# Kernel tuning notes

Hardware: AMD Instinct MI355X
Metric: run time of the kernel (lower is better)

Reference implementation:

```python
import jax, jax.numpy as jnp
import numpy as np

D_MODEL = 2048
NUM_HEADS = 16
HEAD_DIM = D_MODEL // NUM_HEADS  # 128


def setup_inputs() -> dict:
    key = jax.random.key(0)
    ks = jax.random.split(key, 9)
    s = 0.02
    x = jax.random.normal(ks[0], (2, 2048, D_MODEL), dtype=jnp.float32)
    Wq = jax.random.normal(ks[1], (D_MODEL, D_MODEL), dtype=jnp.float32) * s
    bq = jnp.zeros((D_MODEL,), dtype=jnp.float32)
    Wk = jax.random.normal(ks[2], (D_MODEL, HEAD_DIM), dtype=jnp.float32) * s
    bk = jnp.zeros((HEAD_DIM,), dtype=jnp.float32)
    Wv = jax.random.normal(ks[3], (D_MODEL, HEAD_DIM), dtype=jnp.float32) * s
    bv = jnp.zeros((HEAD_DIM,), dtype=jnp.float32)
    Wo = jax.random.normal(ks[4], (D_MODEL, D_MODEL), dtype=jnp.float32) * s
    bo = jnp.zeros((D_MODEL,), dtype=jnp.float32)
    return {"x": x, "Wq": Wq, "bq": bq, "Wk": Wk, "bk": bk,
            "Wv": Wv, "bv": bv, "Wo": Wo, "bo": bo}


def reference(x, Wq, bq, Wk, bk, Wv, bv, Wo, bo):
    B, S, _ = x.shape
    # projections
    q = (x @ Wq + bq).reshape(B, S, NUM_HEADS, HEAD_DIM)  # [B,S,H,d]
    k = x @ Wk + bk  # [B,S,d] shared across heads (MQA)
    v = x @ Wv + bv  # [B,S,d]
    scale = 1.0 / jnp.sqrt(jnp.float32(HEAD_DIM))
    # QK^T with shared K: [B,H,Sq,Sk]
    scores = jnp.einsum('bqhd,bkd->bhqk', q, k) * scale
    attn = jax.nn.softmax(scores, axis=-1)
    # AV with shared V: [B,H,Sq,d]
    out = jnp.einsum('bhqk,bkd->bqhd', attn, v).reshape(B, S, D_MODEL)
    return out @ Wo + bo
```

## Files before the change

kernel.cpp:

```cpp
#include <hip/hip_runtime.h>


typedef __attribute__((ext_vector_type(8))) short short8;
typedef __attribute__((ext_vector_type(4))) float f32x4;
typedef __attribute__((ext_vector_type(4))) unsigned int uint4v;

__device__ __forceinline__ unsigned short f2bf(float f) {
  unsigned int u = __float_as_uint(f);
  u += 0x7FFF + ((u >> 16) & 1);
  return (unsigned short)(u >> 16);
}

__device__ __forceinline__ unsigned int pk2(float a, float b) {
  return (unsigned int)f2bf(a) | ((unsigned int)f2bf(b) << 16);
}

__device__ __forceinline__ void gll16(const void* g, void* lds) {
  __builtin_amdgcn_global_load_lds(
      (const __attribute__((address_space(1))) unsigned int*)g,
      (__attribute__((address_space(3))) unsigned int*)lds, 16, 0, 0);
}

__global__ __launch_bounds__(256) void cvtk(const float* __restrict__ in,
                                            unsigned short* __restrict__ out, int n4) {
  int i = blockIdx.x * blockDim.x + threadIdx.x;
  int stride = gridDim.x * blockDim.x;
  for (; i < n4; i += stride) {
    float4 v = reinterpret_cast<const float4*>(in)[i];
    ushort4 o;
    o.x = f2bf(v.x); o.y = f2bf(v.y); o.z = f2bf(v.z); o.w = f2bf(v.w);
    reinterpret_cast<ushort4*>(out)[i] = o;
  }
}

__global__ __launch_bounds__(256) void tcvt2(const float* __restrict__ W0, const float* __restrict__ W1,
                                             unsigned short* __restrict__ D0, unsigned short* __restrict__ D1,
                                             int K, int N) {
  const float* W = blockIdx.z ? W1 : W0;
  unsigned short* Wt = blockIdx.z ? D1 : D0;
  __shared__ float tile[32][33];
  int n0 = blockIdx.x * 32, k0 = blockIdx.y * 32;
  int tx = threadIdx.x, ty = threadIdx.y;
  #pragma unroll
  for (int i = 0; i < 32; i += 8)
    tile[ty + i][tx] = W[(size_t)(k0 + ty + i) * N + n0 + tx];
  __syncthreads();
  #pragma unroll
  for (int i = 0; i < 32; i += 8)
    Wt[(size_t)(n0 + ty + i) * K + k0 + tx] = f2bf(tile[tx][ty + i]);
}

template <int MODE>
__global__ __launch_bounds__(256)
void gemm_nt(const unsigned short* __restrict__ A, const unsigned short* __restrict__ Bt,
             const float* __restrict__ b0, const float* __restrict__ b1,
             const float* __restrict__ b2,
             void* __restrict__ C, unsigned short* __restrict__ C2,
             unsigned short* __restrict__ C3, int M, int N, int K, float cmul) {
  __shared__ unsigned short lA[128 * 64];
  __shared__ unsigned short lB[128 * 64];
  const int t = threadIdx.x;
  const int lane = t & 63;
  const int w = t >> 6;
  const int wr = w >> 1, wc = w & 1;
  const int r15 = lane & 15, g4 = lane >> 4;
  const int tileM = blockIdx.y * 128;
  const int tileN = blockIdx.x * 128;

  f32x4 acc[4][4];
  #pragma unroll
  for (int i = 0; i < 4; i++)
    #pragma unroll
    for (int j = 0; j < 4; j++) acc[i][j] = (f32x4){0.f, 0.f, 0.f, 0.f};

  const int nkt = K >> 6;
  for (int kt = 0; kt < nkt; ++kt) {
    const int k0 = kt * 64;
    #pragma unroll
    for (int i = 0; i < 4; ++i) {
      int flat = i * 256 + t;
      int row = flat >> 3, gc = flat & 7;
      unsigned lb = (unsigned)(i * 256 + w * 64) * 16;
      gll16(A  + (size_t)(tileM + row) * K + k0 + gc * 8, (char*)lA + lb);
      gll16(Bt + (size_t)(tileN + row) * K + k0 + gc * 8, (char*)lB + lb);
    }
    __syncthreads();
    #pragma unroll
    for (int kk = 0; kk < 2; ++kk) {
      short8 af[4], bf[4];
      #pragma unroll
      for (int mt = 0; mt < 4; ++mt)
        af[mt] = *reinterpret_cast<const short8*>(&lA[(wr * 64 + mt * 16 + r15) * 64 + kk * 32 + g4 * 8]);
      #pragma unroll
      for (int nt = 0; nt < 4; ++nt)
        bf[nt] = *reinterpret_cast<const short8*>(&lB[(wc * 64 + nt * 16 + r15) * 64 + kk * 32 + g4 * 8]);
      #pragma unroll
      for (int mt = 0; mt < 4; ++mt)
        #pragma unroll
        for (int nt = 0; nt < 4; ++nt)
          acc[mt][nt] = __builtin_amdgcn_mfma_f32_16x16x32_bf16(af[mt], bf[nt], acc[mt][nt], 0, 0, 0);
    }
    __syncthreads();
  }

  #pragma unroll
  for (int mt = 0; mt < 4; ++mt) {
    #pragma unroll
    for (int nt = 0; nt < 4; ++nt) {
      int col = tileN + wc * 64 + nt * 16 + r15;
      #pragma unroll
      for (int r = 0; r < 4; ++r) {
        int row = tileM + wr * 64 + mt * 16 + g4 * 4 + r;
        float v = acc[mt][nt][r];
        if (MODE == 1) {
          ((float*)C)[(size_t)row * N + col] = v + b0[col];
        } else {
          if (col < 2048) {
            ((unsigned short*)C)[(size_t)row * 2048 + col] = f2bf((v + b0[col]) * cmul);
          } else if (col < 2176) {
            int dd = col - 2048;
            C2[(size_t)row * 128 + dd] = f2bf(v + b1[dd]);
          } else {
            int dd = col - 2176;
            int bb = row >> 11, s = row & 2047;
            C3[((size_t)bb * 128 + dd) * 2048 + s] = f2bf(v + b2[dd]);
          }
        }
      }
    }
  }
}

__global__ __launch_bounds__(256)
void flash_mqa(const unsigned short* __restrict__ qb, const unsigned short* __restrict__ kb,
               const unsigned short* __restrict__ vt, unsigned short* __restrict__ ob) {
  __shared__ unsigned short lK[2][64 * 128];
  __shared__ unsigned short lV[2][128 * 64];
  __shared__ unsigned short lP[4][16 * 64];

  const int t = threadIdx.x;
  const int lane = t & 63;
  const int w = t >> 6;
  const int r15 = lane & 15, g4 = lane >> 4;
  const int qt = blockIdx.x, hy = blockIdx.y, b = blockIdx.z;
  const int q0 = qt * 64 + w * 16;

  short8 qf[2][4];
  const size_t qrow = (size_t)(b * 2048 + q0 + r15);
  #pragma unroll
  for (int hh = 0; hh < 2; ++hh)
    #pragma unroll
    for (int kk = 0; kk < 4; ++kk)
      qf[hh][kk] = *reinterpret_cast<const short8*>(
          &qb[qrow * 2048 + (hy * 2 + hh) * 128 + kk * 32 + g4 * 8]);

  f32x4 oacc[2][8];
  #pragma unroll
  for (int hh = 0; hh < 2; ++hh)
    #pragma unroll
    for (int i = 0; i < 8; i++) oacc[hh][i] = (f32x4){0.f, 0.f, 0.f, 0.f};
  float m_q[2] = {-1e30f, -1e30f}, l_q[2] = {0.f, 0.f};

  const unsigned short* kbase = kb + (size_t)b * 2048 * 128;
  const unsigned short* vbase = vt + (size_t)b * 128 * 2048;

  auto stage = [&](int buf, int kv0) {
    #pragma unroll
    for (int i = 0; i < 4; ++i) {
      int flat = i * 256 + t;
      unsigned lb = (unsigned)(i * 256 + w * 64) * 16;
      { int row = flat >> 4, gc = flat & 15;
        gll16(kbase + (size_t)(kv0 + row) * 128 + ((gc ^ (row & 15)) << 3), (char*)lK[buf] + lb); }
      { int row = flat >> 3, gc = flat & 7;
        gll16(vbase + (size_t)row * 2048 + kv0 + ((gc ^ (row & 7)) << 3), (char*)lV[buf] + lb); }
    }
  };

  stage(0, 0);
  int cur = 0;
  for (int it = 0; it < 32; ++it) {
    if (it < 31) {
      stage(cur ^ 1, (it + 1) * 64);
      asm volatile("s_waitcnt vmcnt(8)" ::: "memory");
    } else {
      asm volatile("s_waitcnt vmcnt(0)" ::: "memory");
    }
    __builtin_amdgcn_s_barrier();
    asm volatile("" ::: "memory");

    const unsigned short* cK = lK[cur];
    const unsigned short* cV = lV[cur];

    #pragma unroll
    for (int hh = 0; hh < 2; ++hh) {
      f32x4 s[4];
      #pragma unroll
      for (int ct = 0; ct < 4; ct++) s[ct] = (f32x4){0.f, 0.f, 0.f, 0.f};
      #pragma unroll
      for (int kk = 0; kk < 4; ++kk) {
        #pragma unroll
        for (int ct = 0; ct < 4; ++ct) {
          const int krow = ct * 16 + r15;
          const int kg = (kk * 4 + g4) ^ (krow & 15);
          short8 kf = *reinterpret_cast<const short8*>(&cK[krow * 128 + kg * 8]);
          s[ct] = __builtin_amdgcn_mfma_f32_16x16x32_bf16(kf, qf[hh][kk], s[ct], 0, 0, 0);
        }
      }

      float mx = s[0][0];
      #pragma unroll
      for (int ct = 0; ct < 4; ++ct)
        #pragma unroll
        for (int r = 0; r < 4; ++r) mx = fmaxf(mx, s[ct][r]);
      mx = fmaxf(mx, __shfl_xor(mx, 16));
      mx = fmaxf(mx, __shfl_xor(mx, 32));
      if (__any(mx > m_q[hh] + 11.5416f)) {
        float mn = fmaxf(m_q[hh], mx);
        float rf = exp2f(m_q[hh] - mn);
        m_q[hh] = mn;
        l_q[hh] *= rf;
        #pragma unroll
        for (int ot = 0; ot < 8; ++ot)
          #pragma unroll
          for (int r = 0; r < 4; ++r) oacc[hh][ot][r] *= rf;
      }
      #pragma unroll
      for (int ct = 0; ct < 4; ++ct) {
        float p0 = exp2f(s[ct][0] - m_q[hh]);
        float p1 = exp2f(s[ct][1] - m_q[hh]);
        float p2 = exp2f(s[ct][2] - m_q[hh]);
        float p3 = exp2f(s[ct][3] - m_q[hh]);
        l_q[hh] += (p0 + p1) + (p2 + p3);
        const int gi = (ct * 4 + g4) ^ r15;
        *reinterpret_cast<uint2*>(&lP[w][r15 * 64 + gi * 4]) = make_uint2(pk2(p0, p1), pk2(p2, p3));
      }

      #pragma unroll
      for (int kk = 0; kk < 2; ++kk) {
        const int gA = (kk * 8 + g4 * 2) ^ r15;
        const int gB = (kk * 8 + g4 * 2 + 1) ^ r15;
        const uint2 wa = *reinterpret_cast<const uint2*>(&lP[w][r15 * 64 + gA * 4]);
        const uint2 wb = *reinterpret_cast<const uint2*>(&lP[w][r15 * 64 + gB * 4]);
        uint4v pw = {wa.x, wa.y, wb.x, wb.y};
        short8 pf = __builtin_bit_cast(short8, pw);
        #pragma unroll
        for (int ot = 0; ot < 8; ++ot) {
          const int vrow = ot * 16 + r15;
          const int vg = (kk * 4 + g4) ^ (vrow & 7);
          short8 vf = *reinterpret_cast<const short8*>(&cV[vrow * 64 + vg * 8]);
          oacc[hh][ot] = __builtin_amdgcn_mfma_f32_16x16x32_bf16(vf, pf, oacc[hh][ot], 0, 0, 0);
        }
      }
    }

    asm volatile("" ::: "memory");
    __builtin_amdgcn_s_barrier();
    cur ^= 1;
  }

  #pragma unroll
  for (int hh = 0; hh < 2; ++hh) {
    float l = l_q[hh];
    l += __shfl_xor(l, 16);
    l += __shfl_xor(l, 32);
    const float inv = 1.0f / l;
    const int row = q0 + r15;
    const size_t base = ((size_t)(b * 2048 + row)) * 2048 + (hy * 2 + hh) * 128;
    #pragma unroll
    for (int ot = 0; ot < 8; ++ot) {
      uint2 pw = make_uint2(pk2(oacc[hh][ot][0] * inv, oacc[hh][ot][1] * inv),
                            pk2(oacc[hh][ot][2] * inv, oacc[hh][ot][3] * inv));
      *reinterpret_cast<uint2*>(&ob[base + ot * 16 + g4 * 4]) = pw;
    }
  }
}

extern "C" void kernel_launch(void* const* d_in, const int* in_sizes, int n_in,
                              void* d_out, int out_size, void* d_ws, size_t ws_size,
                              hipStream_t stream) {
  const float* x  = (const float*)d_in[0];
  const float* Wq = (const float*)d_in[1];
  const float* bq = (const float*)d_in[2];
  const float* Wk = (const float*)d_in[3];
  const float* bk = (const float*)d_in[4];
  const float* Wv = (const float*)d_in[5];
  const float* bv = (const float*)d_in[6];
  const float* Wo = (const float*)d_in[7];
  const float* bo = (const float*)d_in[8];
  float* out = (float*)d_out;

  char* ws = (char*)d_ws;
  size_t off = 0;
  auto alloc = [&](size_t elems) {
    unsigned short* p = (unsigned short*)(ws + off);
    off += (elems * 2 + 255) & ~(size_t)255;
    return p;
  };
  unsigned short* xb    = alloc(8388608);
  unsigned short* qb    = alloc(8388608);
  unsigned short* ob    = alloc(8388608);
  unsigned short* wqkvt = alloc(4718592);
  unsigned short* wot   = alloc(4194304);
  unsigned short* kbuf  = alloc(524288);
  unsigned short* vtb   = alloc(524288);

  const float qscale = 0.08838834764831845f * 1.44269504088896f;

  dim3 tb(32, 8);
  cvtk<<<4096, 256, 0, stream>>>(x, xb, 2097152);
  tcvt2<<<dim3(64, 64, 2), tb, 0, stream>>>(Wq, Wo, wqkvt, wot, 2048, 2048);
  tcvt2<<<dim3(4, 64, 2),  tb, 0, stream>>>(Wk, Wv, wqkvt + (size_t)2048 * 2048,
                                            wqkvt + (size_t)2176 * 2048, 2048, 128);

  gemm_nt<3><<<dim3(18, 32), 256, 0, stream>>>(xb, wqkvt, bq, bk, bv,
                                               qb, kbuf, vtb, 4096, 2304, 2048, qscale);
  flash_mqa<<<dim3(32, 8, 2), 256, 0, stream>>>(qb, kbuf, vtb, ob);
  gemm_nt<1><<<dim3(16, 32), 256, 0, stream>>>(ob, wot, bo, nullptr, nullptr,
                                               out, nullptr, nullptr, 4096, 2048, 2048, 1.0f);
}
```

Baseline: 287.0 us.

## Double-buffer LDS tiles in GEMM to overlap global loads with MFMA

Turns the GEMM's single LDS buffers for A and B into two-stage ping-pong buffers. The next k-tile is issued via global_load_lds before computing on the current one, and each iteration ends with one vmcnt wait plus a barrier instead of two syncthreads. The aim is to hide global memory latency behind MFMA work. LDS use doubles to 64KB per block, which may lower occupancy. There is also a possible hazard: the next stage's loads could overwrite a buffer that slower waves are still reading.

After: 287.6 us. Within noise of the previous version (+0.2%).

```diff
diff --git a/kernel.cpp b/kernel.cpp
--- a/kernel.cpp
+++ b/kernel.cpp
@@ -57,8 +57,8 @@
              const float* __restrict__ b2,
              void* __restrict__ C, unsigned short* __restrict__ C2,
              unsigned short* __restrict__ C3, int M, int N, int K, float cmul) {
-  __shared__ unsigned short lA[128 * 64];
-  __shared__ unsigned short lB[128 * 64];
+  __shared__ unsigned short lA[2][128 * 64];
+  __shared__ unsigned short lB[2][128 * 64];
   const int t = threadIdx.x;
   const int lane = t & 63;
   const int w = t >> 6;
@@ -73,34 +73,52 @@
     #pragma unroll
     for (int j = 0; j < 4; j++) acc[i][j] = (f32x4){0.f, 0.f, 0.f, 0.f};
 
-  const int nkt = K >> 6;
-  for (int kt = 0; kt < nkt; ++kt) {
+  auto stage = [&](int buf, int kt) {
     const int k0 = kt * 64;
     #pragma unroll
     for (int i = 0; i < 4; ++i) {
       int flat = i * 256 + t;
       int row = flat >> 3, gc = flat & 7;
       unsigned lb = (unsigned)(i * 256 + w * 64) * 16;
-      gll16(A  + (size_t)(tileM + row) * K + k0 + gc * 8, (char*)lA + lb);
-      gll16(Bt + (size_t)(tileN + row) * K + k0 + gc * 8, (char*)lB + lb);
-    }
-    __syncthreads();
+      gll16(A  + (size_t)(tileM + row) * K + k0 + gc * 8, (char*)lA[buf] + lb);
+      gll16(Bt + (size_t)(tileN + row) * K + k0 + gc * 8, (char*)lB[buf] + lb);
+    }
+  };
+
+  const int nkt = K >> 6;
+  stage(0, 0);
+  asm volatile("s_waitcnt vmcnt(0)" ::: "memory");
+  __builtin_amdgcn_s_barrier();
+  asm volatile("" ::: "memory");
+
+  int cur = 0;
+  for (int kt = 0; kt < nkt; ++kt) {
+    if (kt + 1 < nkt) stage(cur ^ 1, kt + 1);
+
+    const unsigned short* cA = lA[cur];
+    const unsigned short* cB = lB[cur];
     #pragma unroll
     for (int kk = 0; kk < 2; ++kk) {
       short8 af[4], bf[4];
       #pragma unroll
       for (int mt = 0; mt < 4; ++mt)
-        af[mt] = *reinterpret_cast<const short8*>(&lA[(wr * 64 + mt * 16 + r15) * 64 + kk * 32 + g4 * 8]);
+        af[mt] = *reinterpret_cast<const short8*>(&cA[(wr * 64 + mt * 16 + r15) * 64 + kk * 32 + g4 * 8]);
       #pragma unroll
       for (int nt = 0; nt < 4; ++nt)
-        bf[nt] = *reinterpret_cast<const short8*>(&lB[(wc * 64 + nt * 16 + r15) * 64 + kk * 32 + g4 * 8]);
+        bf[nt] = *reinterpret_cast<const short8*>(&cB[(wc * 64 + nt * 16 + r15) * 64 + kk * 32 + g4 * 8]);
       #pragma unroll
       for (int mt = 0; mt < 4; ++mt)
         #pragma unroll
         for (int nt = 0; nt < 4; ++nt)
           acc[mt][nt] = __builtin_amdgcn_mfma_f32_16x16x32_bf16(af[mt], bf[nt], acc[mt][nt], 0, 0, 0);
     }
-    __syncthreads();
+
+    if (kt + 1 < nkt) {
+      asm volatile("s_waitcnt vmcnt(0)" ::: "memory");
+      __builtin_amdgcn_s_barrier();
+      asm volatile("" ::: "memory");
+    }
+    cur ^= 1;
   }
 
   #pragma unroll
```

## Merge prep kernels into one launch and enlarge GEMM tiles to 256x128

Applied to the files above, without the earlier changes.

Folds the x conversion and the two weight transpose-convert launches into a single prep kernel dispatched by block id, removing two kernel launches. The GEMM now uses 512-thread blocks covering 256x128 output tiles, so each B tile in LDS serves twice as many rows. It also replaces __syncthreads with an explicit vmcnt wait plus s_barrier. Larger tiles halve the grid and raise LDS use per block, which lowers the number of blocks and may reduce occupancy on a GPU with many CUs.

Result: no change. 284.8 us (-0.8%).

```diff
diff --git a/kernel.cpp b/kernel.cpp
--- a/kernel.cpp
+++ b/kernel.cpp
@@ -21,26 +21,46 @@
       (__attribute__((address_space(3))) unsigned int*)lds, 16, 0, 0);
 }
 
-__global__ __launch_bounds__(256) void cvtk(const float* __restrict__ in,
-                                            unsigned short* __restrict__ out, int n4) {
-  int i = blockIdx.x * blockDim.x + threadIdx.x;
-  int stride = gridDim.x * blockDim.x;
-  for (; i < n4; i += stride) {
-    float4 v = reinterpret_cast<const float4*>(in)[i];
-    ushort4 o;
-    o.x = f2bf(v.x); o.y = f2bf(v.y); o.z = f2bf(v.z); o.w = f2bf(v.w);
-    reinterpret_cast<ushort4*>(out)[i] = o;
-  }
-}
-
-__global__ __launch_bounds__(256) void tcvt2(const float* __restrict__ W0, const float* __restrict__ W1,
-                                             unsigned short* __restrict__ D0, unsigned short* __restrict__ D1,
-                                             int K, int N) {
-  const float* W = blockIdx.z ? W1 : W0;
-  unsigned short* Wt = blockIdx.z ? D1 : D0;
+__global__ __launch_bounds__(256)
+void prep(const float* __restrict__ x, unsigned short* __restrict__ xb,
+          const float* __restrict__ Wq, const float* __restrict__ Wo,
+          const float* __restrict__ Wk, const float* __restrict__ Wv,
+          unsigned short* __restrict__ wqkvt, unsigned short* __restrict__ wot) {
   __shared__ float tile[32][33];
-  int n0 = blockIdx.x * 32, k0 = blockIdx.y * 32;
-  int tx = threadIdx.x, ty = threadIdx.y;
+  const int bid = blockIdx.x;
+  const int t = threadIdx.x;
+
+  if (bid < 4096) {
+    int i = bid * 256 + t;
+    const int stride = 4096 * 256;
+    #pragma unroll
+    for (int rep = 0; rep < 2; ++rep, i += stride) {
+      float4 v = reinterpret_cast<const float4*>(x)[i];
+      ushort4 o;
+      o.x = f2bf(v.x); o.y = f2bf(v.y); o.z = f2bf(v.z); o.w = f2bf(v.w);
+      reinterpret_cast<ushort4*>(xb)[i] = o;
+    }
+    return;
+  }
+
+  const float* W;
+  unsigned short* Wt;
+  int K = 2048, N, bx, by;
+  if (bid < 12288) {
+    int r = bid - 4096;
+    int z = r >> 12, rr = r & 4095;
+    bx = rr & 63; by = rr >> 6; N = 2048;
+    W = z ? Wo : Wq;
+    Wt = z ? wot : wqkvt;
+  } else {
+    int r = bid - 12288;
+    int z = r >> 8, rr = r & 255;
+    bx = rr & 3; by = rr >> 2; N = 128;
+    W = z ? Wv : Wk;
+    Wt = wqkvt + (size_t)(z ? 2176 : 2048) * 2048;
+  }
+  const int tx = t & 31, ty = t >> 5;
+  const int n0 = bx * 32, k0 = by * 32;
   #pragma unroll
   for (int i = 0; i < 32; i += 8)
     tile[ty + i][tx] = W[(size_t)(k0 + ty + i) * N + n0 + tx];
@@ -51,20 +71,20 @@
 }
 
 template <int MODE>
-__global__ __launch_bounds__(256)
+__global__ __launch_bounds__(512, 4)
 void gemm_nt(const unsigned short* __restrict__ A, const unsigned short* __restrict__ Bt,
              const float* __restrict__ b0, const float* __restrict__ b1,
              const float* __restrict__ b2,
              void* __restrict__ C, unsigned short* __restrict__ C2,
              unsigned short* __restrict__ C3, int M, int N, int K, float cmul) {
-  __shared__ unsigned short lA[128 * 64];
+  __shared__ unsigned short lA[256 * 64];
   __shared__ unsigned short lB[128 * 64];
   const int t = threadIdx.x;
   const int lane = t & 63;
   const int w = t >> 6;
   const int wr = w >> 1, wc = w & 1;
   const int r15 = lane & 15, g4 = lane >> 4;
-  const int tileM = blockIdx.y * 128;
+  const int tileM = blockIdx.y * 256;
   const int tileN = blockIdx.x * 128;
 
   f32x4 acc[4][4];
@@ -78,13 +98,22 @@
     const int k0 = kt * 64;
     #pragma unroll
     for (int i = 0; i < 4; ++i) {
-      int flat = i * 256 + t;
+      int flat = i * 512 + t;
       int row = flat >> 3, gc = flat & 7;
-      unsigned lb = (unsigned)(i * 256 + w * 64) * 16;
-      gll16(A  + (size_t)(tileM + row) * K + k0 + gc * 8, (char*)lA + lb);
+      unsigned lb = (unsigned)(i * 512 + w * 64) * 16;
+      gll16(A + (size_t)(tileM + row) * K + k0 + gc * 8, (char*)lA + lb);
+    }
+    #pragma unroll
+    for (int i = 0; i < 2; ++i) {
+      int flat = i * 512 + t;
+      int row = flat >> 3, gc = flat & 7;
+      unsigned lb = (unsigned)(i * 512 + w * 64) * 16;
       gll16(Bt + (size_t)(tileN + row) * K + k0 + gc * 8, (char*)lB + lb);
     }
-    __syncthreads();
+    asm volatile("s_waitcnt vmcnt(0)" ::: "memory");
+    __builtin_amdgcn_s_barrier();
+    asm volatile("" ::: "memory");
+
     #pragma unroll
     for (int kk = 0; kk < 2; ++kk) {
       short8 af[4], bf[4];
@@ -100,7 +129,8 @@
         for (int nt = 0; nt < 4; ++nt)
           acc[mt][nt] = __builtin_amdgcn_mfma_f32_16x16x32_bf16(af[mt], bf[nt], acc[mt][nt], 0, 0, 0);
     }
-    __syncthreads();
+    asm volatile("" ::: "memory");
+    __builtin_amdgcn_s_barrier();
   }
 
   #pragma unroll
@@ -306,15 +336,11 @@
 
   const float qscale = 0.08838834764831845f * 1.44269504088896f;
 
-  dim3 tb(32, 8);
-  cvtk<<<4096, 256, 0, stream>>>(x, xb, 2097152);
-  tcvt2<<<dim3(64, 64, 2), tb, 0, stream>>>(Wq, Wo, wqkvt, wot, 2048, 2048);
-  tcvt2<<<dim3(4, 64, 2),  tb, 0, stream>>>(Wk, Wv, wqkvt + (size_t)2048 * 2048,
-                                            wqkvt + (size_t)2176 * 2048, 2048, 128);
-
-  gemm_nt<3><<<dim3(18, 32), 256, 0, stream>>>(xb, wqkvt, bq, bk, bv,
+  prep<<<12800, 256, 0, stream>>>(x, xb, Wq, Wo, Wk, Wv, wqkvt, wot);
+
+  gemm_nt<3><<<dim3(18, 16), 512, 0, stream>>>(xb, wqkvt, bq, bk, bv,
                                                qb, kbuf, vtb, 4096, 2304, 2048, qscale);
   flash_mqa<<<dim3(32, 8, 2), 256, 0, stream>>>(qb, kbuf, vtb, ob);
-  gemm_nt<1><<<dim3(16, 32), 256, 0, stream>>>(ob, wot, bo, nullptr, nullptr,
+  gemm_nt<1><<<dim3(16, 16), 512, 0, stream>>>(ob, wot, bo, nullptr, nullptr,
                                                out, nullptr, nullptr, 4096, 2048, 2048, 1.0f);
 }
```
